# Optimization experiments

Hardware: AMD Instinct MI355X
Metric: run time of the kernel (lower is better)

Reference implementation:

```python
import jax, jax.numpy as jnp
import numpy as np
import math

N = 4264          # all_node_num
B = 256           # batch size
VIS = 784 + 50    # input_node_num + label_node_num
NG = 8            # number of color groups (Pegasus chromatic number is small)
GS = N // NG      # 533 nodes per group
SAMPLE_NUM = 10   # Gibbs sweeps (default 1000 in source; reduced for reference)
AVG_DEG = 15.0    # Pegasus graph degree ~15


def setup_inputs() -> dict:
    key = jax.random.key(0)
    k1, k2, k3, k4 = jax.random.split(key, 4)
    # spin state in {-1, +1}, shape [B, N]
    m = jnp.where(jax.random.normal(k1, (B, N)) >= 0, 1.0, -1.0).astype(jnp.float32)
    # sparse symmetric coupling matrix J: ~AVG_DEG neighbors per node, values randn*0.01
    upper_mask = jnp.triu(jax.random.uniform(k2, (N, N)) < (AVG_DEG / N), k=1)
    Jup = jax.random.normal(k3, (N, N), dtype=jnp.float32) * 0.01 * upper_mask
    J = Jup + Jup.T
    # bias H: log-odds constant on visible nodes, zero on hidden
    h_vis = math.log((VIS / N) / (1.0 - VIS / N))
    H = jnp.zeros((N,), dtype=jnp.float32).at[:VIS].set(h_vis)
    # color groups: disjoint partition of node indices, [NG, GS]
    groups = jax.random.permutation(k4, N).reshape(NG, GS).astype(jnp.int32)
    return {"m": m, "J": J, "H": H, "groups": groups, "sample_num": SAMPLE_NUM}


def reference(m, J, H, groups, sample_num):
    n_groups = groups.shape[0]

    def sweep(m, key):
        keys = jax.random.split(key, n_groups)
        for g in range(n_groups):          # small fixed set of color groups
            idx = groups[g]                # [GS]
            # I = sparse.mm(J[idx], m.T).T + H[idx]  ->  [B, GS]
            I = jnp.einsum('bn,gn->bg', m, J[idx]) + H[idx]
            r = jax.random.uniform(keys[g], I.shape, dtype=I.dtype) * 2.0 - 1.0
            m = m.at[:, idx].set(jnp.sign(jnp.tanh(I) - r))
        return m, None

    iter_keys = jax.random.split(jax.random.key(42), sample_num)
    m, _ = jax.lax.scan(sweep, m, iter_keys)
    return m
```

## Files before the change

kernel.cpp:

```cpp
#include <hip/hip_runtime.h>
#include <hip/hip_bf16.h>
#include <stdint.h>

#define NN 4264
#define BB 256
#define GSZ 533
#define NGRP 8
#define NSWEEP 10
#define NSTEP (NSWEEP * NGRP)
#define DMAX 48
#define DFIX 24
#define NF4 1066
#define NIT 17
#define GW (GSZ * DFIX)
#define SLABW 12800
#define NCH 50

struct Keys { unsigned k0[NSTEP]; unsigned k1[NSTEP]; };

#define TF_ROUND(x0, x1, r) { x0 += x1; x1 = (x1 << (r)) | (x1 >> (32 - (r))); x1 ^= x0; }
#define TF_BODY(K0, K1, C0, C1, O0, O1) {                                   \
  unsigned ks0 = (K0), ks1 = (K1), ks2 = (K0) ^ (K1) ^ 0x1BD11BDAu;          \
  unsigned x0 = (C0) + ks0, x1 = (C1) + ks1;                                 \
  TF_ROUND(x0, x1, 13) TF_ROUND(x0, x1, 15) TF_ROUND(x0, x1, 26) TF_ROUND(x0, x1, 6)  \
  x0 += ks1; x1 += ks2 + 1u;                                                 \
  TF_ROUND(x0, x1, 17) TF_ROUND(x0, x1, 29) TF_ROUND(x0, x1, 16) TF_ROUND(x0, x1, 24) \
  x0 += ks2; x1 += ks0 + 2u;                                                 \
  TF_ROUND(x0, x1, 13) TF_ROUND(x0, x1, 15) TF_ROUND(x0, x1, 26) TF_ROUND(x0, x1, 6)  \
  x0 += ks0; x1 += ks1 + 3u;                                                 \
  TF_ROUND(x0, x1, 17) TF_ROUND(x0, x1, 29) TF_ROUND(x0, x1, 16) TF_ROUND(x0, x1, 24) \
  x0 += ks1; x1 += ks2 + 4u;                                                 \
  TF_ROUND(x0, x1, 13) TF_ROUND(x0, x1, 15) TF_ROUND(x0, x1, 26) TF_ROUND(x0, x1, 6)  \
  x0 += ks2; x1 += ks0 + 5u;                                                 \
  (O0) = x0; (O1) = x1; }

static void tf_host(unsigned k0, unsigned k1, unsigned c0, unsigned c1,
                    unsigned* o0, unsigned* o1) {
  unsigned a, b;
  TF_BODY(k0, k1, c0, c1, a, b);
  *o0 = a; *o1 = b;
}

__device__ __forceinline__ void tf_dev(unsigned k0, unsigned k1, unsigned c0, unsigned c1,
                                       unsigned& o0, unsigned& o1) {
  TF_BODY(k0, k1, c0, c1, o0, o1);
}

__device__ __forceinline__ float tf_r(unsigned k0, unsigned k1, unsigned c) {
  unsigned o0, o1;
  tf_dev(k0, k1, 0u, c, o0, o1);
  const unsigned bits = o0 ^ o1;
  const float u = __uint_as_float((bits >> 9) | 0x3f800000u) - 1.0f;
  return u * 2.0f - 1.0f;
}

__global__ __launch_bounds__(256) void build_ell(const float* __restrict__ J,
                                                 const int* __restrict__ groups,
                                                 unsigned* __restrict__ pack4,
                                                 int2* __restrict__ exact8,
                                                 int* __restrict__ deg,
                                                 float* __restrict__ marg) {
  const int wv = threadIdx.x >> 6, lane = threadIdx.x & 63;
  const int p = blockIdx.x * 4 + wv;
  if (p >= NN) return;
  const int g = p / GSZ;
  const int ii = p - g * GSZ;
  unsigned* pg = pack4 + (size_t)g * GW;
  const int node = groups[p];
  const float4* row = (const float4*)(J + (size_t)node * NN);

  float4 vv[NIT];
#pragma unroll
  for (int it = 0; it < NIT; ++it) {
    const int q = it * 64 + lane;
    vv[it] = (q < NF4) ? row[q] : make_float4(0.0f, 0.0f, 0.0f, 0.0f);
  }

  int cnt = 0;
  float asum = 0.0f;
#pragma unroll
  for (int it = 0; it < NIT; ++it) {
    const float4 v = vv[it];
    const int c0 = (it * 64 + lane) * 4;
#define COMP(X, CIDX) {                                                        \
      const bool nz = ((X) != 0.0f);                                           \
      const unsigned long long mk = __ballot(nz);                              \
      const int rk = cnt + __popcll(mk & ((1ull << lane) - 1ull));             \
      if (nz) {                                                                \
        if (rk < DFIX) {                                                       \
          const unsigned bits = __float_as_uint(X);                            \
          const unsigned bf = (bits + 0x7fffu + ((bits >> 16) & 1u)) >> 16;    \
          pg[(size_t)rk * GSZ + ii] = (bf << 16) | ((unsigned)(CIDX) << 2);    \
          asum += fabsf(X);                                                    \
        }                                                                      \
        if (rk < DMAX)                                                         \
          exact8[(size_t)p * DMAX + rk] = make_int2((CIDX), __float_as_int(X));\
      }                                                                        \
      cnt += __popcll(mk); }
    COMP(v.x, c0 + 0) COMP(v.y, c0 + 1) COMP(v.z, c0 + 2) COMP(v.w, c0 + 3)
#undef COMP
  }
  for (int k = cnt + lane; k < DFIX; k += 64) pg[(size_t)k * GSZ + ii] = 0u;
  for (int s = 1; s < 64; s <<= 1) asum += __shfl_xor(asum, s, 64);
  if (lane == 0) {
    deg[p] = (cnt > DMAX) ? DMAX : cnt;
    marg[p] = asum * 0.001953125f + 2e-5f;
  }
}

__global__ __launch_bounds__(576, 3) void gibbs(const float* __restrict__ m0,
                                                const float* __restrict__ H,
                                                const int* __restrict__ groups,
                                                const unsigned* __restrict__ pack4,
                                                const int2* __restrict__ exact8,
                                                const int* __restrict__ deg,
                                                const float* __restrict__ marg,
                                                float* __restrict__ out,
                                                Keys keys) {
  __shared__ float m_lds[NN];
  __shared__ unsigned pbuf[2][SLABW];
  const int b = blockIdx.x;
  const int i = threadIdx.x;
  const int wv = i >> 6, lane = i & 63;
  const bool active = (i < GSZ);

  for (int n = i; n < NN; n += 576) m_lds[n] = m0[(size_t)b * NN + n];

#define STAGE(GN, BUF) {                                                        \
    const char* gbase = (const char*)pack4 + (size_t)(GN) * (GW * 4);           \
    char* lbase = (char*)(&pbuf[(BUF)][0]);                                     \
    for (int ch = wv; ch < NCH; ch += 9) {                                      \
      __builtin_amdgcn_global_load_lds(                                         \
          (const __attribute__((address_space(1))) unsigned*)(gbase + ch * 1024 + lane * 16), \
          (__attribute__((address_space(3))) unsigned*)(lbase + ch * 1024 + lane * 16),       \
          16, 0, 0);                                                            \
    }                                                                           \
  }
  STAGE(0, 0)

  int nodeg[NGRP];
  float hg[NGRP], mgg[NGRP];
  int dgg[NGRP];
  if (active) {
#pragma unroll
    for (int g = 0; g < NGRP; ++g) {
      const int p = g * GSZ + i;
      nodeg[g] = groups[p];
      hg[g] = H[nodeg[g]];
      dgg[g] = deg[p];
      mgg[g] = marg[p];
    }
  }

  const unsigned c = (unsigned)(b * GSZ + i);
  float rcur = 0.0f, Acur = 0.0f;
  if (active) {
    rcur = tf_r(keys.k0[0], keys.k1[0], c);
    Acur = 0.5f * logf((1.0f + rcur) / (1.0f - rcur));
  }
  __syncthreads();

#pragma unroll 1
  for (int t = 0; t < NSWEEP; ++t) {
#pragma unroll
    for (int g = 0; g < NGRP; ++g) {
      const int step = t * NGRP + g;
      const int cur = step & 1;
      STAGE((g + 1) & (NGRP - 1), cur ^ 1)

      float nv = 0.0f;
      float rnext = 0.0f, Anext = 0.0f;
      if (active) {
        {
          const int sn = (step + 1 < NSTEP) ? step + 1 : step;
          rnext = tf_r(keys.k0[sn], keys.k1[sn], c);
          Anext = 0.5f * logf((1.0f + rnext) / (1.0f - rnext));
        }

        const unsigned* pb = pbuf[cur];
        float a0 = 0.0f, a1 = 0.0f, a2 = 0.0f, a3 = 0.0f;
#define MV(W)  (*(const float*)((const char*)m_lds + ((W) & 0xFFFCu)))
#pragma unroll
        for (int k = 0; k < DFIX; k += 4) {
          const unsigned e0 = pb[(k + 0) * GSZ + i];
          const unsigned e1 = pb[(k + 1) * GSZ + i];
          const unsigned e2 = pb[(k + 2) * GSZ + i];
          const unsigned e3 = pb[(k + 3) * GSZ + i];
          a0 += __uint_as_float(e0 & 0xFFFF0000u) * MV(e0);
          a1 += __uint_as_float(e1 & 0xFFFF0000u) * MV(e1);
          a2 += __uint_as_float(e2 & 0xFFFF0000u) * MV(e2);
          a3 += __uint_as_float(e3 & 0xFFFF0000u) * MV(e3);
        }
#undef MV
        const int dg = dgg[g];
        if (__builtin_expect(dg > DFIX, 0)) {
          const int2* ep = exact8 + (size_t)(g * GSZ + i) * DMAX;
          for (int k = DFIX; k < dg; ++k) {
            const int2 e = ep[k];
            a0 += __int_as_float(e.y) * m_lds[e.x];
          }
        }
        const float I = ((a0 + a1) + (a2 + a3)) + hg[g];

        const float d = I - Acur;
        if (__builtin_expect(fabsf(d) > mgg[g], 1)) {
          nv = (d > 0.0f) ? 1.0f : -1.0f;
        } else {
          const int2* ep = exact8 + (size_t)(g * GSZ + i) * DMAX;
          double I64 = (double)hg[g];
          for (int k = 0; k < dg; ++k) {
            const int2 e = ep[k];
            I64 += (double)__int_as_float(e.y) * (double)m_lds[e.x];
          }
          const double diff = tanh(I64) - (double)rcur;
          nv = (diff > 0.0) ? 1.0f : ((diff < 0.0) ? -1.0f : 0.0f);
        }
      }
      __syncthreads();
      if (active) m_lds[nodeg[g]] = nv;
      __syncthreads();
      rcur = rnext; Acur = Anext;
    }
  }

  for (int n = i; n < NN; n += 576) out[(size_t)b * NN + n] = m_lds[n];
#undef STAGE
}

extern "C" void kernel_launch(void* const* d_in, const int* in_sizes, int n_in,
                              void* d_out, int out_size, void* d_ws, size_t ws_size,
                              hipStream_t stream) {
  const float* m0     = (const float*)d_in[0];
  const float* J      = (const float*)d_in[1];
  const float* H      = (const float*)d_in[2];
  const int*   groups = (const int*)d_in[3];

  char* ws = (char*)d_ws;
  unsigned* pack4  = (unsigned*)ws;                     ws += (size_t)NGRP * GW * 4 + 64;
  int2*     exact8 = (int2*)ws;                         ws += (size_t)NN * DMAX * 8;
  int*      deg    = (int*)ws;                          ws += (size_t)NN * 4;
  float*    marg   = (float*)ws;

  Keys keys;
  for (int t = 0; t < NSWEEP; ++t) {
    unsigned ik0, ik1;
    tf_host(0u, 42u, 0u, (unsigned)t, &ik0, &ik1);
    for (int g = 0; g < NGRP; ++g) {
      unsigned gk0, gk1;
      tf_host(ik0, ik1, 0u, (unsigned)g, &gk0, &gk1);
      keys.k0[t * NGRP + g] = gk0;
      keys.k1[t * NGRP + g] = gk1;
    }
  }

  build_ell<<<(NN + 3) / 4, 256, 0, stream>>>(J, groups, pack4, exact8, deg, marg);
  gibbs<<<BB, 576, 0, stream>>>(m0, H, groups, pack4, exact8, deg, marg,
                                (float*)d_out, keys);
}
```

Baseline: 316.6 us.

## Precompute random thresholds in massively parallel prep kernel and stream them via LDS

```diff
diff --git a/kernel.cpp b/kernel.cpp
--- a/kernel.cpp
+++ b/kernel.cpp
@@ -8,6 +8,7 @@
 #define NGRP 8
 #define NSWEEP 10
 #define NSTEP (NSWEEP * NGRP)
+#define NTOT (BB * GSZ)
 #define DMAX 48
 #define DFIX 24
 #define NF4 1066
@@ -15,6 +16,8 @@
 #define GW (GSZ * DFIX)
 #define SLABW 12800
 #define NCH 50
+#define AWRDS 576
+#define NBBUILD ((NN + 3) / 4)
 
 struct Keys { unsigned k0[NSTEP]; unsigned k1[NSTEP]; };
 
@@ -54,12 +57,23 @@
   return u * 2.0f - 1.0f;
 }
 
-__global__ __launch_bounds__(256) void build_ell(const float* __restrict__ J,
-                                                 const int* __restrict__ groups,
-                                                 unsigned* __restrict__ pack4,
-                                                 int2* __restrict__ exact8,
-                                                 int* __restrict__ deg,
-                                                 float* __restrict__ marg) {
+__global__ __launch_bounds__(256) void prep(const float* __restrict__ J,
+                                            const int* __restrict__ groups,
+                                            unsigned* __restrict__ pack4,
+                                            float* __restrict__ Atab,
+                                            int2* __restrict__ exact8,
+                                            int* __restrict__ deg,
+                                            float* __restrict__ marg,
+                                            Keys keys) {
+  if (blockIdx.x >= NBBUILD) {
+    const int idx = blockIdx.x - NBBUILD;
+    const int step = idx / GSZ;
+    const int chunk = idx % GSZ;
+    const unsigned c = (unsigned)(chunk * 256 + threadIdx.x);
+    const float r = tf_r(keys.k0[step], keys.k1[step], c);
+    Atab[(size_t)step * NTOT + c] = 0.5f * logf((1.0f + r) / (1.0f - r));
+    return;
+  }
   const int wv = threadIdx.x >> 6, lane = threadIdx.x & 63;
   const int p = blockIdx.x * 4 + wv;
   if (p >= NN) return;
@@ -108,10 +122,12 @@
   }
 }
 
+template <bool USE_A>
 __global__ __launch_bounds__(576, 3) void gibbs(const float* __restrict__ m0,
                                                 const float* __restrict__ H,
                                                 const int* __restrict__ groups,
                                                 const unsigned* __restrict__ pack4,
+                                                const float* __restrict__ Atab,
                                                 const int2* __restrict__ exact8,
                                                 const int* __restrict__ deg,
                                                 const float* __restrict__ marg,
@@ -119,6 +135,7 @@
                                                 Keys keys) {
   __shared__ float m_lds[NN];
   __shared__ unsigned pbuf[2][SLABW];
+  __shared__ float abuf[2][AWRDS];
   const int b = blockIdx.x;
   const int i = threadIdx.x;
   const int wv = i >> 6, lane = i & 63;
@@ -136,7 +153,19 @@
           16, 0, 0);                                                            \
     }                                                                           \
   }
+#define STAGE_A(SN, BUF) if (USE_A) {                                           \
+    const char* gA = (const char*)Atab + ((size_t)(SN) * NTOT + (size_t)b * GSZ) * 4; \
+    char* lA = (char*)(&abuf[(BUF)][0]);                                        \
+    if (wv < 9) {                                                               \
+      __builtin_amdgcn_global_load_lds(                                         \
+          (const __attribute__((address_space(1))) unsigned*)(gA + wv * 256 + lane * 4),  \
+          (__attribute__((address_space(3))) unsigned*)(lA + wv * 256 + lane * 4),        \
+          4, 0, 0);                                                             \
+    }                                                                           \
+  }
+
   STAGE(0, 0)
+  STAGE_A(0, 0)
 
   int nodeg[NGRP];
   float hg[NGRP], mgg[NGRP];
@@ -151,13 +180,7 @@
       mgg[g] = marg[p];
     }
   }
-
   const unsigned c = (unsigned)(b * GSZ + i);
-  float rcur = 0.0f, Acur = 0.0f;
-  if (active) {
-    rcur = tf_r(keys.k0[0], keys.k1[0], c);
-    Acur = 0.5f * logf((1.0f + rcur) / (1.0f - rcur));
-  }
   __syncthreads();
 
 #pragma unroll 1
@@ -167,16 +190,13 @@
       const int step = t * NGRP + g;
       const int cur = step & 1;
       STAGE((g + 1) & (NGRP - 1), cur ^ 1)
+      {
+        const int sn = (step + 1 < NSTEP) ? step + 1 : step;
+        STAGE_A(sn, cur ^ 1)
+      }
 
       float nv = 0.0f;
-      float rnext = 0.0f, Anext = 0.0f;
       if (active) {
-        {
-          const int sn = (step + 1 < NSTEP) ? step + 1 : step;
-          rnext = tf_r(keys.k0[sn], keys.k1[sn], c);
-          Anext = 0.5f * logf((1.0f + rnext) / (1.0f - rnext));
-        }
-
         const unsigned* pb = pbuf[cur];
         float a0 = 0.0f, a1 = 0.0f, a2 = 0.0f, a3 = 0.0f;
 #define MV(W)  (*(const float*)((const char*)m_lds + ((W) & 0xFFFCu)))
@@ -202,29 +222,35 @@
         }
         const float I = ((a0 + a1) + (a2 + a3)) + hg[g];
 
-        const float d = I - Acur;
+        float d;
+        if (USE_A) {
+          d = I - abuf[cur][i];
+        } else {
+          d = tanhf(I) - tf_r(keys.k0[step], keys.k1[step], c);
+        }
         if (__builtin_expect(fabsf(d) > mgg[g], 1)) {
           nv = (d > 0.0f) ? 1.0f : -1.0f;
         } else {
+          const float r = tf_r(keys.k0[step], keys.k1[step], c);
           const int2* ep = exact8 + (size_t)(g * GSZ + i) * DMAX;
           double I64 = (double)hg[g];
           for (int k = 0; k < dg; ++k) {
             const int2 e = ep[k];
             I64 += (double)__int_as_float(e.y) * (double)m_lds[e.x];
           }
-          const double diff = tanh(I64) - (double)rcur;
+          const double diff = tanh(I64) - (double)r;
           nv = (diff > 0.0) ? 1.0f : ((diff < 0.0) ? -1.0f : 0.0f);
         }
       }
       __syncthreads();
       if (active) m_lds[nodeg[g]] = nv;
       __syncthreads();
-      rcur = rnext; Acur = Anext;
     }
   }
 
   for (int n = i; n < NN; n += 576) out[(size_t)b * NN + n] = m_lds[n];
 #undef STAGE
+#undef STAGE_A
 }
 
 extern "C" void kernel_launch(void* const* d_in, const int* in_sizes, int n_in,
@@ -237,9 +263,11 @@
 
   char* ws = (char*)d_ws;
   unsigned* pack4  = (unsigned*)ws;                     ws += (size_t)NGRP * GW * 4 + 64;
+  float*    Atab   = (float*)ws;                        ws += (size_t)NSTEP * NTOT * 4;
   int2*     exact8 = (int2*)ws;                         ws += (size_t)NN * DMAX * 8;
   int*      deg    = (int*)ws;                          ws += (size_t)NN * 4;
-  float*    marg   = (float*)ws;
+  float*    marg   = (float*)ws;                        ws += (size_t)NN * 4;
+  const bool use_a = ((size_t)(ws - (char*)d_ws) <= ws_size);
 
   Keys keys;
   for (int t = 0; t < NSWEEP; ++t) {
@@ -253,7 +281,15 @@
     }
   }
 
-  build_ell<<<(NN + 3) / 4, 256, 0, stream>>>(J, groups, pack4, exact8, deg, marg);
-  gibbs<<<BB, 576, 0, stream>>>(m0, H, groups, pack4, exact8, deg, marg,
-                                (float*)d_out, keys);
-}
+  if (use_a) {
+    prep<<<NBBUILD + NSTEP * GSZ, 256, 0, stream>>>(J, groups, pack4, Atab,
+                                                    exact8, deg, marg, keys);
+    gibbs<true><<<BB, 576, 0, stream>>>(m0, H, groups, pack4, Atab, exact8,
+                                        deg, marg, (float*)d_out, keys);
+  } else {
+    prep<<<NBBUILD, 256, 0, stream>>>(J, groups, pack4, Atab,
+                                      exact8, deg, marg, keys);
+    gibbs<false><<<BB, 576, 0, stream>>>(m0, H, groups, pack4, Atab, exact8,
+                                         deg, marg, (float*)d_out, keys);
+  }
+}
```

Measured after the change: 338.4 us. 6.9% more time.
